# Optimization experiments

Hardware: AMD Instinct MI355X
Metric: run time of the kernel (lower is better)

## Reference

```python
import jax, jax.numpy as jnp
import numpy as np

NH = 16      # num_attention_heads
NKV = 8      # num_key_value_heads
G = NH // NKV  # num_key_value_groups
D = 128      # head_dim = hidden_size // NH
ROPE_MAX = 2048


def _rope_tables(seq_len, dtype=jnp.float32):
    # matches RotaryEmbedding: inv_freq over even dims, freqs duplicated (concat), cos/sin cached
    inv_freq = 1.0 / (10000.0 ** (jnp.arange(0, D, 2, dtype=jnp.float32) / D))
    t = jnp.arange(ROPE_MAX, dtype=jnp.float32)[:, None]          # [max, 1]
    freqs = t * inv_freq[None, :]                                  # [max, D/2]
    freqs = jnp.concatenate((freqs, freqs), axis=-1)               # [max, D]
    cos = jnp.cos(freqs)[:seq_len].astype(dtype)                   # [S, D]
    sin = jnp.sin(freqs)[:seq_len].astype(dtype)
    # unsqueeze(0) then unsqueeze(2) -> [1, S, 1, D] broadcasting over batch and heads
    return cos[None, :, None, :], sin[None, :, None, :]


def _rotate_half(x):
    x1, x2 = jnp.split(x, 2, axis=-1)
    return jnp.concatenate((-x2, x1), axis=-1)


def setup_inputs() -> dict:
    key = jax.random.key(0)
    ks = jax.random.split(key, 5)
    B, S, H = 2, 2048, 2048
    scale = 1.0 / np.sqrt(H)
    return {
        "hidden_states": jax.random.normal(ks[0], (B, S, H), jnp.float32),
        "Wq": jax.random.normal(ks[1], (H, H), jnp.float32) * scale,
        "Wk": jax.random.normal(ks[2], (NKV * D, H), jnp.float32) * scale,
        "Wv": jax.random.normal(ks[3], (NKV * D, H), jnp.float32) * scale,
        "Wo": jax.random.normal(ks[4], (H, H), jnp.float32) * scale,
    }


def reference(hidden_states, Wq, Wk, Wv, Wo):
    B, S, H = hidden_states.shape
    # projections (nn.Linear: y = x @ W.T, no bias)
    q = (hidden_states @ Wq.T).reshape(B, S, NH, D)     # [B,S,NH,D]
    k = (hidden_states @ Wk.T).reshape(B, S, NKV, D)    # [B,S,NKV,D]
    v = (hidden_states @ Wv.T).reshape(B, S, NKV, D)

    cos, sin = _rope_tables(S, hidden_states.dtype)
    q = q * cos + _rotate_half(q) * sin
    k = k * cos + _rotate_half(k) * sin

    # GQA: query head h attends to kv head h // G (repeat_kv ordering: h = n*G + g)
    qg = q.reshape(B, S, NKV, G, D).transpose(0, 2, 3, 1, 4)   # [B,NKV,G,S,D]
    kt = k.transpose(0, 2, 1, 3)                                # [B,NKV,S,D]
    vt = v.transpose(0, 2, 1, 3)                                # [B,NKV,S,D]

    scores = jnp.einsum("bngqd,bnkd->bngqk", qg, kt) / np.sqrt(D)  # [B,NKV,G,S,S]
    causal = jnp.triu(jnp.ones((S, S), dtype=bool), k=1)
    neg = jnp.finfo(scores.dtype).min
    scores = jnp.where(causal[None, None, None], neg, scores)
    probs = jax.nn.softmax(scores.astype(jnp.float32), axis=-1).astype(q.dtype)

    out = jnp.einsum("bngqk,bnkd->bngqd", probs, vt)            # [B,NKV,G,S,D]
    out = out.transpose(0, 3, 1, 2, 4).reshape(B, S, H)         # [B,S,H]
    return out @ Wo.T
```

## Files before the change

kernel.cpp:

```cpp
#include <hip/hip_runtime.h>

typedef unsigned short u16;
typedef __attribute__((ext_vector_type(8))) short short8;
typedef __attribute__((ext_vector_type(4))) float f32x4;

__device__ __forceinline__ u16 f2bf(float f) {
  unsigned u = __float_as_uint(f);
  return (u16)((u + 0x7FFFu + ((u >> 16) & 1u)) >> 16);
}
__device__ __forceinline__ float bf2f(u16 h) {
  return __uint_as_float(((unsigned)h) << 16);
}

__device__ __forceinline__ void gload_lds16(const void* g, void* l) {
  __builtin_amdgcn_global_load_lds(
      (const __attribute__((address_space(1))) unsigned*)g,
      (__attribute__((address_space(3))) unsigned*)l, 16, 0, 0);
}

__global__ void cast_f32_bf16_k(const float4* __restrict__ in, u16* __restrict__ out, int n4) {
  int i = blockIdx.x * 256 + threadIdx.x;
  if (i >= n4) return;
  float4 v = in[i];
  union { u16 u[4]; uint2 d; } r;
  r.u[0] = f2bf(v.x); r.u[1] = f2bf(v.y); r.u[2] = f2bf(v.z); r.u[3] = f2bf(v.w);
  *reinterpret_cast<uint2*>(out + (size_t)i * 4) = r.d;
}

__global__ void rope_tables_k(float* __restrict__ cosT, float* __restrict__ sinT) {
  int idx = blockIdx.x * 256 + threadIdx.x;
  int i = idx & 63, s = idx >> 6;
  double inv = pow(10000.0, -(double)(2 * i) / 128.0);
  double f = (double)s * inv;
  cosT[idx] = (float)cos(f);
  sinT[idx] = (float)sin(f);
}

__global__ void rope_q_k(u16* __restrict__ x, const float* __restrict__ cosT,
                         const float* __restrict__ sinT) {
  int idx = blockIdx.x * 256 + threadIdx.x;
  int i = idx & 63;
  int hh = (idx >> 6) & 15;
  int row = idx >> 10;
  int s = row & 2047;
  size_t base = (size_t)row * 4096 + hh * 128;
  float x1 = bf2f(x[base + i]);
  float x2 = bf2f(x[base + i + 64]);
  float c = cosT[s * 64 + i], sn = sinT[s * 64 + i];
  x[base + i]      = f2bf(x1 * c - x2 * sn);
  x[base + i + 64] = f2bf(x2 * c + x1 * sn);
}

__global__ void rope_repack_k_k(const u16* __restrict__ qkv, u16* __restrict__ kt,
                                const float* __restrict__ cosT, const float* __restrict__ sinT) {
  int idx = blockIdx.x * 256 + threadIdx.x;
  int i = idx & 63;
  int kvh = (idx >> 6) & 7;
  int row = idx >> 9;
  int s = row & 2047, b = row >> 11;
  size_t src = (size_t)row * 4096 + 2048 + kvh * 128;
  float x1 = bf2f(qkv[src + i]);
  float x2 = bf2f(qkv[src + i + 64]);
  float c = cosT[s * 64 + i], sn = sinT[s * 64 + i];
  size_t dst = ((size_t)(b * 8 + kvh) * 2048 + s) * 128;
  kt[dst + i]      = f2bf(x1 * c - x2 * sn);
  kt[dst + i + 64] = f2bf(x2 * c + x1 * sn);
}

__global__ void transpose_v_k(const u16* __restrict__ qkv, u16* __restrict__ vt) {
  __shared__ u16 tile[128][129];
  int bn = blockIdx.y;
  int s0 = blockIdx.x * 128;
  int b = bn >> 3, n = bn & 7;
  for (int e = threadIdx.x; e < 128 * 128; e += 256) {
    int r = e >> 7, c = e & 127;
    tile[r][c] = qkv[(size_t)(b * 2048 + s0 + r) * 4096 + 3072 + n * 128 + c];
  }
  __syncthreads();
  for (int e = threadIdx.x; e < 128 * 128; e += 256) {
    int r = e >> 7, c = e & 127;
    vt[((size_t)bn * 128 + r) * 2048 + s0 + c] = tile[c][r];
  }
}

template<typename OutT>
__global__ __launch_bounds__(256) void gemm_bt_k(
    const u16* __restrict__ A, const u16* __restrict__ Bm,
    OutT* __restrict__ C, int M, int N, int K)
{
  __shared__ __align__(16) u16 As[128 * 32];
  __shared__ __align__(16) u16 Bs[128 * 32];
  const int tid = threadIdx.x;
  const int wave = tid >> 6, lane = tid & 63;
  const int wr = wave >> 1, wc = wave & 1;
  const int lrow = lane & 15, lgrp = lane >> 4;
  const int nwg = (int)(gridDim.x * gridDim.y);
  const int f = (int)(blockIdx.y * gridDim.x + blockIdx.x);
  const int sw = (f & 7) * (nwg >> 3) + (f >> 3);
  const int bx = sw % gridDim.x, by = sw / gridDim.x;
  const int row0 = by * 128, col0 = bx * 128;

  f32x4 acc[4][4];
  #pragma unroll
  for (int m = 0; m < 4; ++m)
    #pragma unroll
    for (int n = 0; n < 4; ++n) acc[m][n] = (f32x4){0.f, 0.f, 0.f, 0.f};

  for (int k0 = 0; k0 < K; k0 += 32) {
    #pragma unroll
    for (int i = 0; i < 2; ++i) {
      int c = i * 256 + tid;
      int r = c >> 2, cc = (c & 3) * 8;
      gload_lds16(A + (size_t)(row0 + r) * K + k0 + cc,
                  As + (size_t)(i * 256 + wave * 64) * 8);
      gload_lds16(Bm + (size_t)(col0 + r) * K + k0 + cc,
                  Bs + (size_t)(i * 256 + wave * 64) * 8);
    }
    __syncthreads();
    short8 af[4], bfr[4];
    #pragma unroll
    for (int m = 0; m < 4; ++m)
      af[m] = *reinterpret_cast<const short8*>(As + (wr * 64 + m * 16 + lrow) * 32 + lgrp * 8);
    #pragma unroll
    for (int n = 0; n < 4; ++n)
      bfr[n] = *reinterpret_cast<const short8*>(Bs + (wc * 64 + n * 16 + lrow) * 32 + lgrp * 8);
    #pragma unroll
    for (int m = 0; m < 4; ++m)
      #pragma unroll
      for (int n = 0; n < 4; ++n)
        acc[m][n] = __builtin_amdgcn_mfma_f32_16x16x32_bf16(af[m], bfr[n], acc[m][n], 0, 0, 0);
    __syncthreads();
  }
  #pragma unroll
  for (int m = 0; m < 4; ++m)
    #pragma unroll
    for (int n = 0; n < 4; ++n)
      #pragma unroll
      for (int j = 0; j < 4; ++j) {
        int r = row0 + wr * 64 + m * 16 + lgrp * 4 + j;
        int col = col0 + wc * 64 + n * 16 + lrow;
        float val = acc[m][n][j];
        if constexpr (sizeof(OutT) == 2) C[(size_t)r * N + col] = f2bf(val);
        else                             C[(size_t)r * N + col] = val;
      }
}

template<typename OutT>
__global__ __launch_bounds__(512, 1) void gemm256_k(
    const u16* __restrict__ A, const u16* __restrict__ Bm,
    OutT* __restrict__ C, int M, int N, int K)
{
  __shared__ __align__(16) u16 As[2][256 * 64];
  __shared__ __align__(16) u16 Bs[2][256 * 64];
  const int tid = threadIdx.x;
  const int wave = tid >> 6, lane = tid & 63;
  const int wm = wave >> 2, wn = wave & 3;
  const int lrow = lane & 15, lgrp = lane >> 4;
  const int gx = (int)gridDim.x;
  const int nwg = gx * (int)gridDim.y;
  const int f = (int)(blockIdx.y * gridDim.x + blockIdx.x);
  const int sw = (f & 7) * (nwg >> 3) + (f >> 3);
  const int bx = sw % gx, by = sw / gx;
  const int row0 = by * 256, col0 = bx * 256;

  f32x4 acc[8][4];
  #pragma unroll
  for (int m = 0; m < 8; ++m)
    #pragma unroll
    for (int n = 0; n < 4; ++n) acc[m][n] = (f32x4){0.f, 0.f, 0.f, 0.f};

  const int NT = K >> 6;

  auto stage = [&](int buf, int k0) {
    #pragma unroll
    for (int i = 0; i < 4; ++i) {
      int cid = i * 512 + tid;
      int row = cid >> 3, cp = cid & 7;
      int c = cp ^ (row & 7);
      gload_lds16(A + (size_t)(row0 + row) * K + k0 + c * 8,
                  &As[buf][(size_t)(i * 512 + wave * 64) * 8]);
      gload_lds16(Bm + (size_t)(col0 + row) * K + k0 + c * 8,
                  &Bs[buf][(size_t)(i * 512 + wave * 64) * 8]);
    }
  };

  stage(0, 0);
  for (int t = 0; t < NT; ++t) {
    const int cur = t & 1;
    if (t + 1 < NT) {
      stage(cur ^ 1, (t + 1) << 6);
      asm volatile("s_waitcnt vmcnt(8)" ::: "memory");
    } else {
      asm volatile("s_waitcnt vmcnt(0)" ::: "memory");
    }
    __builtin_amdgcn_s_barrier();
    __builtin_amdgcn_sched_barrier(0);
    #pragma unroll
    for (int ks = 0; ks < 2; ++ks) {
      short8 af[8], bfr[4];
      #pragma unroll
      for (int m = 0; m < 8; ++m) {
        int row = wm * 128 + m * 16 + lrow;
        int cp = (ks * 4 + lgrp) ^ (row & 7);
        af[m] = *reinterpret_cast<const short8*>(&As[cur][row * 64 + cp * 8]);
      }
      #pragma unroll
      for (int n = 0; n < 4; ++n) {
        int row = wn * 64 + n * 16 + lrow;
        int cp = (ks * 4 + lgrp) ^ (row & 7);
        bfr[n] = *reinterpret_cast<const short8*>(&Bs[cur][row * 64 + cp * 8]);
      }
      #pragma unroll
      for (int m = 0; m < 8; ++m)
        #pragma unroll
        for (int n = 0; n < 4; ++n)
          acc[m][n] = __builtin_amdgcn_mfma_f32_16x16x32_bf16(af[m], bfr[n], acc[m][n], 0, 0, 0);
    }
    __builtin_amdgcn_sched_barrier(0);
    __builtin_amdgcn_s_barrier();
  }

  #pragma unroll
  for (int m = 0; m < 8; ++m)
    #pragma unroll
    for (int n = 0; n < 4; ++n)
      #pragma unroll
      for (int j = 0; j < 4; ++j) {
        int r = row0 + wm * 128 + m * 16 + lgrp * 4 + j;
        int col = col0 + wn * 64 + n * 16 + lrow;
        float val = acc[m][n][j];
        if constexpr (sizeof(OutT) == 2) C[(size_t)r * N + col] = f2bf(val);
        else                             C[(size_t)r * N + col] = val;
      }
}

__global__ __launch_bounds__(256, 2) void flash_attn_k(
    const u16* __restrict__ qkv, const u16* __restrict__ kt,
    const u16* __restrict__ vt, u16* __restrict__ o)
{
  constexpr int S = 2048, NH = 16, NKV = 8, D = 128;
  const int wave = threadIdx.x >> 6, lane = threadIdx.x & 63;
  const int flat = blockIdx.x;
  const int g = flat >> 5;
  const int qtile = (g < 8) ? (15 - g) : (g - 8);
  const int bh = (flat & 7) * 4 + ((flat >> 3) & 3);
  const int b = bh >> 4, h = bh & 15;
  const int kvh = h >> 1;
  const int q0 = qtile * 128 + wave * 32;
  const int lrow = lane & 15, lgrp = lane >> 4;

  __shared__ __align__(16) u16 ks[2][64 * 128];
  __shared__ __align__(16) u16 vs[2][128 * 64];

  short8 qf[2][4];
  #pragma unroll
  for (int rg = 0; rg < 2; ++rg) {
    const u16* qbase = qkv + (size_t)(b * S + q0 + rg * 16 + lrow) * 4096 + h * 128;
    #pragma unroll
    for (int kc = 0; kc < 4; ++kc)
      qf[rg][kc] = *reinterpret_cast<const short8*>(qbase + kc * 32 + lgrp * 8);
  }

  f32x4 acc[2][8];
  #pragma unroll
  for (int rg = 0; rg < 2; ++rg)
    #pragma unroll
    for (int n = 0; n < 8; ++n) acc[rg][n] = (f32x4){0.f, 0.f, 0.f, 0.f};
  float l_part[2][4] = {{0.f,0.f,0.f,0.f},{0.f,0.f,0.f,0.f}};

  const float scale = 0.08838834764831845f;
  const u16* khead = kt + (size_t)(b * NKV + kvh) * S * D;
  const u16* vhead = vt + (size_t)(b * NKV + kvh) * D * S;
  const int trips = (qtile + 1) * 2;

  auto stage = [&](int nxt, int kv0n) {
    #pragma unroll
    for (int i = 0; i < 4; ++i) {
      int c = i * 256 + wave * 64 + lane;
      int kr = c >> 4;
      int kc16 = (c & 15) ^ (kr & 7);
      gload_lds16(khead + (size_t)(kv0n + kr) * D + kc16 * 8,
                  &ks[nxt][(size_t)(i * 256 + wave * 64) * 8]);
      int vr = c >> 3;
      int vc = (c & 7) ^ (vr & 7);
      gload_lds16(vhead + (size_t)vr * S + kv0n + vc * 8,
                  &vs[nxt][(size_t)(i * 256 + wave * 64) * 8]);
    }
  };

  stage(0, 0);
  __syncthreads();

  for (int t = 0; t < trips; ++t) {
    const int cur = t & 1;
    const int kv0 = t * 64;
    const bool active = kv0 < q0 + 32;
    f32x4 sc[2][4];
    if (active) {
      #pragma unroll
      for (int rg = 0; rg < 2; ++rg)
        #pragma unroll
        for (int nb = 0; nb < 4; ++nb) sc[rg][nb] = (f32x4){0.f, 0.f, 0.f, 0.f};
      #pragma unroll
      for (int nb = 0; nb < 4; ++nb) {
        const int r = nb * 16 + lrow;
        short8 kf[4];
        #pragma unroll
        for (int kc = 0; kc < 4; ++kc) {
          int ch = (kc * 4 + lgrp) ^ (r & 7);
          kf[kc] = *reinterpret_cast<const short8*>(&ks[cur][r * 128 + ch * 8]);
        }
        #pragma unroll
        for (int rg = 0; rg < 2; ++rg)
          #pragma unroll
          for (int kc = 0; kc < 4; ++kc)
            sc[rg][nb] = __builtin_amdgcn_mfma_f32_16x16x32_bf16(qf[rg][kc], kf[kc], sc[rg][nb], 0, 0, 0);
      }
    }
    __syncthreads();
    if (t + 1 < trips) stage(cur ^ 1, kv0 + 64);
    if (active) {
      u16* pb = &ks[cur][wave * 2048];
      #pragma unroll
      for (int rg = 0; rg < 2; ++rg)
        #pragma unroll
        for (int nb = 0; nb < 4; ++nb) {
          int kv_idx = kv0 + nb * 16 + lrow;
          #pragma unroll
          for (int j = 0; j < 4; ++j) {
            int qr = rg * 16 + lgrp * 4 + j;
            int q_idx = q0 + qr;
            float sv = fminf(sc[rg][nb][j] * scale, 30.f);
            float p = (kv_idx <= q_idx) ? __expf(sv) : 0.f;
            l_part[rg][j] += p;
            pb[qr * 64 + ((nb * 16 + lrow) ^ ((qr & 7) << 3))] = f2bf(p);
          }
        }
      short8 pf[2][2];
      #pragma unroll
      for (int rg = 0; rg < 2; ++rg)
        #pragma unroll
        for (int kc2 = 0; kc2 < 2; ++kc2) {
          int r = rg * 16 + lrow;
          int ch = (kc2 * 4 + lgrp) ^ (r & 7);
          pf[rg][kc2] = *reinterpret_cast<const short8*>(&pb[r * 64 + ch * 8]);
        }
      #pragma unroll
      for (int n = 0; n < 8; ++n) {
        const int d = n * 16 + lrow;
        #pragma unroll
        for (int kc2 = 0; kc2 < 2; ++kc2) {
          int ch = (kc2 * 4 + lgrp) ^ (d & 7);
          short8 vf = *reinterpret_cast<const short8*>(&vs[cur][d * 64 + ch * 8]);
          #pragma unroll
          for (int rg = 0; rg < 2; ++rg)
            acc[rg][n] = __builtin_amdgcn_mfma_f32_16x16x32_bf16(pf[rg][kc2], vf, acc[rg][n], 0, 0, 0);
        }
      }
    }
    __syncthreads();
  }

  #pragma unroll
  for (int rg = 0; rg < 2; ++rg) {
    float inv[4];
    #pragma unroll
    for (int j = 0; j < 4; ++j) {
      float s = l_part[rg][j];
      #pragma unroll
      for (int off = 8; off; off >>= 1) s += __shfl_xor(s, off);
      inv[j] = 1.f / s;
    }
    u16* obase = o + (((size_t)(b * S + q0 + rg * 16)) * NH + h) * D;
    #pragma unroll
    for (int n = 0; n < 8; ++n)
      #pragma unroll
      for (int j = 0; j < 4; ++j)
        obase[(size_t)(lgrp * 4 + j) * NH * D + n * 16 + lrow] = f2bf(acc[rg][n][j] * inv[j]);
  }
}

extern "C" void kernel_launch(void* const* d_in, const int* in_sizes, int n_in,
                              void* d_out, int out_size, void* d_ws, size_t ws_size,
                              hipStream_t stream) {
  const float* hs = (const float*)d_in[0];
  const float* Wq = (const float*)d_in[1];
  const float* Wk = (const float*)d_in[2];
  const float* Wv = (const float*)d_in[3];
  const float* Wo = (const float*)d_in[4];
  float* out = (float*)d_out;

  constexpr int B = 2, S = 2048, H = 2048, NH = 16, NKV = 8, D = 128;
  constexpr int M = B * S;
  constexpr int NQKV = 4096;

  char* w = (char*)d_ws;
  auto alloc = [&](size_t bytes) { char* p = w; w += (bytes + 255) & ~(size_t)255; return p; };
  u16* hs_bf   = (u16*)alloc((size_t)M * H * 2);
  u16* wqkv_bf = (u16*)alloc((size_t)NQKV * H * 2);
  u16* wo_bf   = (u16*)alloc((size_t)H * H * 2);
  u16* qkv     = (u16*)alloc((size_t)M * NQKV * 2);
  float* cosT  = (float*)alloc((size_t)S * 64 * 4);
  float* sinT  = (float*)alloc((size_t)S * 64 * 4);
  u16* attn = hs_bf;
  u16* vt   = wqkv_bf;
  u16* kt   = wqkv_bf + (size_t)B * NKV * D * S;

  cast_f32_bf16_k<<<(M * H / 4) / 256, 256, 0, stream>>>((const float4*)hs, hs_bf, M * H / 4);
  cast_f32_bf16_k<<<(H * H / 4) / 256, 256, 0, stream>>>((const float4*)Wq, wqkv_bf, H * H / 4);
  cast_f32_bf16_k<<<(NKV * D * H / 4) / 256, 256, 0, stream>>>((const float4*)Wk, wqkv_bf + (size_t)2048 * H, NKV * D * H / 4);
  cast_f32_bf16_k<<<(NKV * D * H / 4) / 256, 256, 0, stream>>>((const float4*)Wv, wqkv_bf + (size_t)3072 * H, NKV * D * H / 4);
  cast_f32_bf16_k<<<(H * H / 4) / 256, 256, 0, stream>>>((const float4*)Wo, wo_bf, H * H / 4);
  rope_tables_k<<<(S * 64) / 256, 256, 0, stream>>>(cosT, sinT);

  gemm256_k<u16><<<dim3(NQKV / 256, M / 256), 512, 0, stream>>>(hs_bf, wqkv_bf, qkv, M, NQKV, H);

  rope_q_k<<<(M * 16 * 64) / 256, 256, 0, stream>>>(qkv, cosT, sinT);
  rope_repack_k_k<<<(M * 8 * 64) / 256, 256, 0, stream>>>(qkv, kt, cosT, sinT);
  transpose_v_k<<<dim3(S / 128, B * NKV), 256, 0, stream>>>(qkv, vt);

  flash_attn_k<<<512, 256, 0, stream>>>(qkv, kt, vt, attn);

  gemm_bt_k<float><<<dim3(H / 128, M / 128), 256, 0, stream>>>(attn, wo_bf, out, M, H, H);
}
```

Baseline: 253.1 us.

## Pair causal 64-row query tiles per block and swizzle GEMM LDS reads

The flash attention kernel now handles two 64-row query tiles per block, a long one (31-pr) and a short one (pr), processed one after the other. Each wave owns 16 query rows, so the per-tile inactive-wave masking is gone and causal work is more even across blocks. Exponentials switch to exp2f with a log2e-folded scale. The GEMM kernel also XOR-swizzles its LDS tile columns to reduce bank conflicts. In exchange, each wave's MFMA work per staged K/V tile drops by half, so loads and barriers are amortised over fewer instructions.

```diff
diff --git a/kernel.cpp b/kernel.cpp
--- a/kernel.cpp
+++ b/kernel.cpp
@@ -110,7 +110,7 @@
     #pragma unroll
     for (int i = 0; i < 2; ++i) {
       int c = i * 256 + tid;
-      int r = c >> 2, cc = (c & 3) * 8;
+      int r = c >> 2, cc = ((c & 3) ^ (r & 3)) * 8;
       gload_lds16(A + (size_t)(row0 + r) * K + k0 + cc,
                   As + (size_t)(i * 256 + wave * 64) * 8);
       gload_lds16(Bm + (size_t)(col0 + r) * K + k0 + cc,
@@ -120,10 +120,10 @@
     short8 af[4], bfr[4];
     #pragma unroll
     for (int m = 0; m < 4; ++m)
-      af[m] = *reinterpret_cast<const short8*>(As + (wr * 64 + m * 16 + lrow) * 32 + lgrp * 8);
+      af[m] = *reinterpret_cast<const short8*>(As + (wr * 64 + m * 16 + lrow) * 32 + (lgrp ^ (lrow & 3)) * 8);
     #pragma unroll
     for (int n = 0; n < 4; ++n)
-      bfr[n] = *reinterpret_cast<const short8*>(Bs + (wc * 64 + n * 16 + lrow) * 32 + lgrp * 8);
+      bfr[n] = *reinterpret_cast<const short8*>(Bs + (wc * 64 + n * 16 + lrow) * 32 + (lgrp ^ (lrow & 3)) * 8);
     #pragma unroll
     for (int m = 0; m < 4; ++m)
       #pragma unroll
@@ -241,37 +241,18 @@
   constexpr int S = 2048, NH = 16, NKV = 8, D = 128;
   const int wave = threadIdx.x >> 6, lane = threadIdx.x & 63;
   const int flat = blockIdx.x;
-  const int g = flat >> 5;
-  const int qtile = (g < 8) ? (15 - g) : (g - 8);
+  const int pr = flat >> 5;
   const int bh = (flat & 7) * 4 + ((flat >> 3) & 3);
   const int b = bh >> 4, h = bh & 15;
   const int kvh = h >> 1;
-  const int q0 = qtile * 128 + wave * 32;
   const int lrow = lane & 15, lgrp = lane >> 4;
 
   __shared__ __align__(16) u16 ks[2][64 * 128];
   __shared__ __align__(16) u16 vs[2][128 * 64];
 
-  short8 qf[2][4];
-  #pragma unroll
-  for (int rg = 0; rg < 2; ++rg) {
-    const u16* qbase = qkv + (size_t)(b * S + q0 + rg * 16 + lrow) * 4096 + h * 128;
-    #pragma unroll
-    for (int kc = 0; kc < 4; ++kc)
-      qf[rg][kc] = *reinterpret_cast<const short8*>(qbase + kc * 32 + lgrp * 8);
-  }
-
-  f32x4 acc[2][8];
-  #pragma unroll
-  for (int rg = 0; rg < 2; ++rg)
-    #pragma unroll
-    for (int n = 0; n < 8; ++n) acc[rg][n] = (f32x4){0.f, 0.f, 0.f, 0.f};
-  float l_part[2][4] = {{0.f,0.f,0.f,0.f},{0.f,0.f,0.f,0.f}};
-
-  const float scale = 0.08838834764831845f;
+  const float scl2 = 0.12754245006443634f;
   const u16* khead = kt + (size_t)(b * NKV + kvh) * S * D;
   const u16* vhead = vt + (size_t)(b * NKV + kvh) * D * S;
-  const int trips = (qtile + 1) * 2;
 
   auto stage = [&](int nxt, int kv0n) {
     #pragma unroll
@@ -288,63 +269,63 @@
     }
   };
 
-  stage(0, 0);
-  __syncthreads();
-
-  for (int t = 0; t < trips; ++t) {
-    const int cur = t & 1;
-    const int kv0 = t * 64;
-    const bool active = kv0 < q0 + 32;
-    f32x4 sc[2][4];
-    if (active) {
-      #pragma unroll
-      for (int rg = 0; rg < 2; ++rg)
-        #pragma unroll
-        for (int nb = 0; nb < 4; ++nb) sc[rg][nb] = (f32x4){0.f, 0.f, 0.f, 0.f};
+  #pragma unroll
+  for (int ph = 0; ph < 2; ++ph) {
+    const int qt = ph ? pr : (31 - pr);
+    const int q0 = qt * 64 + wave * 16;
+    const int trips = qt + 1;
+
+    short8 qf[4];
+    const u16* qbase = qkv + (size_t)(b * S + q0 + lrow) * 4096 + h * 128;
+    #pragma unroll
+    for (int kc = 0; kc < 4; ++kc)
+      qf[kc] = *reinterpret_cast<const short8*>(qbase + kc * 32 + lgrp * 8);
+
+    f32x4 acc[8];
+    #pragma unroll
+    for (int n = 0; n < 8; ++n) acc[n] = (f32x4){0.f, 0.f, 0.f, 0.f};
+    float l_part[4] = {0.f, 0.f, 0.f, 0.f};
+
+    stage(0, 0);
+    __syncthreads();
+
+    for (int t = 0; t < trips; ++t) {
+      const int cur = t & 1;
+      const int kv0 = t * 64;
+      f32x4 sc[4];
       #pragma unroll
       for (int nb = 0; nb < 4; ++nb) {
+        sc[nb] = (f32x4){0.f, 0.f, 0.f, 0.f};
         const int r = nb * 16 + lrow;
-        short8 kf[4];
         #pragma unroll
         for (int kc = 0; kc < 4; ++kc) {
           int ch = (kc * 4 + lgrp) ^ (r & 7);
-          kf[kc] = *reinterpret_cast<const short8*>(&ks[cur][r * 128 + ch * 8]);
+          short8 kf = *reinterpret_cast<const short8*>(&ks[cur][r * 128 + ch * 8]);
+          sc[nb] = __builtin_amdgcn_mfma_f32_16x16x32_bf16(qf[kc], kf, sc[nb], 0, 0, 0);
         }
+      }
+      __syncthreads();
+      if (t + 1 < trips) stage(cur ^ 1, kv0 + 64);
+      u16* pb = &ks[cur][wave * 1024];
+      #pragma unroll
+      for (int nb = 0; nb < 4; ++nb) {
+        int kv_idx = kv0 + nb * 16 + lrow;
         #pragma unroll
-        for (int rg = 0; rg < 2; ++rg)
-          #pragma unroll
-          for (int kc = 0; kc < 4; ++kc)
-            sc[rg][nb] = __builtin_amdgcn_mfma_f32_16x16x32_bf16(qf[rg][kc], kf[kc], sc[rg][nb], 0, 0, 0);
-      }
-    }
-    __syncthreads();
-    if (t + 1 < trips) stage(cur ^ 1, kv0 + 64);
-    if (active) {
-      u16* pb = &ks[cur][wave * 2048];
-      #pragma unroll
-      for (int rg = 0; rg < 2; ++rg)
-        #pragma unroll
-        for (int nb = 0; nb < 4; ++nb) {
-          int kv_idx = kv0 + nb * 16 + lrow;
-          #pragma unroll
-          for (int j = 0; j < 4; ++j) {
-            int qr = rg * 16 + lgrp * 4 + j;
-            int q_idx = q0 + qr;
-            float sv = fminf(sc[rg][nb][j] * scale, 30.f);
-            float p = (kv_idx <= q_idx) ? __expf(sv) : 0.f;
-            l_part[rg][j] += p;
-            pb[qr * 64 + ((nb * 16 + lrow) ^ ((qr & 7) << 3))] = f2bf(p);
-          }
+        for (int j = 0; j < 4; ++j) {
+          int qr = lgrp * 4 + j;
+          int q_idx = q0 + qr;
+          float sv = fminf(sc[nb][j] * scl2, 43.f);
+          float p = (kv_idx <= q_idx) ? exp2f(sv) : 0.f;
+          l_part[j] += p;
+          pb[qr * 64 + ((nb * 16 + lrow) ^ ((qr & 7) << 3))] = f2bf(p);
         }
-      short8 pf[2][2];
-      #pragma unroll
-      for (int rg = 0; rg < 2; ++rg)
-        #pragma unroll
-        for (int kc2 = 0; kc2 < 2; ++kc2) {
-          int r = rg * 16 + lrow;
-          int ch = (kc2 * 4 + lgrp) ^ (r & 7);
-          pf[rg][kc2] = *reinterpret_cast<const short8*>(&pb[r * 64 + ch * 8]);
-        }
+      }
+      short8 pf[2];
+      #pragma unroll
+      for (int kc2 = 0; kc2 < 2; ++kc2) {
+        int ch = (kc2 * 4 + lgrp) ^ (lrow & 7);
+        pf[kc2] = *reinterpret_cast<const short8*>(&pb[lrow * 64 + ch * 8]);
+      }
       #pragma unroll
       for (int n = 0; n < 8; ++n) {
         const int d = n * 16 + lrow;
@@ -352,31 +333,27 @@
         for (int kc2 = 0; kc2 < 2; ++kc2) {
           int ch = (kc2 * 4 + lgrp) ^ (d & 7);
           short8 vf = *reinterpret_cast<const short8*>(&vs[cur][d * 64 + ch * 8]);
-          #pragma unroll
-          for (int rg = 0; rg < 2; ++rg)
-            acc[rg][n] = __builtin_amdgcn_mfma_f32_16x16x32_bf16(pf[rg][kc2], vf, acc[rg][n], 0, 0, 0);
+          acc[n] = __builtin_amdgcn_mfma_f32_16x16x32_bf16(pf[kc2], vf, acc[n], 0, 0, 0);
         }
       }
-    }
-    __syncthreads();
-  }
-
-  #pragma unroll
-  for (int rg = 0; rg < 2; ++rg) {
+      __syncthreads();
+    }
+
     float inv[4];
     #pragma unroll
     for (int j = 0; j < 4; ++j) {
-      float s = l_part[rg][j];
+      float s = l_part[j];
       #pragma unroll
       for (int off = 8; off; off >>= 1) s += __shfl_xor(s, off);
       inv[j] = 1.f / s;
     }
-    u16* obase = o + (((size_t)(b * S + q0 + rg * 16)) * NH + h) * D;
+    u16* obase = o + (((size_t)(b * S + q0)) * NH + h) * D;
     #pragma unroll
     for (int n = 0; n < 8; ++n)
       #pragma unroll
       for (int j = 0; j < 4; ++j)
-        obase[(size_t)(lgrp * 4 + j) * NH * D + n * 16 + lrow] = f2bf(acc[rg][n][j] * inv[j]);
+        obase[(size_t)(lgrp * 4 + j) * NH * D + n * 16 + lrow] = f2bf(acc[n][j] * inv[j]);
+    __syncthreads();
   }
 }
 
```

Measured after the change: 243.9 us. -3.6%, faster.
